# Kernel tuning notes

Hardware: AMD Instinct MI355X
Metric: run time of the kernel (lower is better)

Reference implementation:

```python
import jax, jax.numpy as jnp
import numpy as np

N = 50000
E = 1_600_000
IN = 256
OUT = 16
NEG_SLOPE = 0.2  # PyG GATConv default leaky_relu slope
EPS = 1e-16


def gat_conv(x, src, dst, W, a_src, a_dst, bias, heads, ch, concat, n_nodes):
    # Linear transform: [N, heads, ch]
    xl = (x @ W).reshape(n_nodes, heads, ch)
    # Per-node attention logits (PyG factorization of a^T [Wx_i || Wx_j])
    alpha_src = jnp.einsum('nhc,hc->nh', xl, a_src)  # [N, H]
    alpha_dst = jnp.einsum('nhc,hc->nh', xl, a_dst)  # [N, H]
    # Per-edge raw attention
    alpha = jax.nn.leaky_relu(alpha_src[src] + alpha_dst[dst], NEG_SLOPE)  # [E, H]
    # Segment softmax over incoming edges of each destination node
    amax = jax.ops.segment_max(alpha, dst, num_segments=n_nodes)  # [N, H]
    alpha = jnp.exp(alpha - amax[dst])
    denom = jax.ops.segment_sum(alpha, dst, num_segments=n_nodes)  # [N, H]
    alpha = alpha / jnp.maximum(denom[dst], EPS)
    # Weighted aggregation of source features
    msg = xl[src] * alpha[:, :, None]  # [E, H, C]
    out = jax.ops.segment_sum(msg, dst, num_segments=n_nodes)  # [N, H, C]
    out = out.reshape(n_nodes, heads * ch) if concat else out.mean(axis=1)
    return out + bias


def setup_inputs() -> dict:
    key = jax.random.key(0)
    ks = jax.random.split(key, 10)
    x = jax.random.normal(ks[0], (N, IN), dtype=jnp.float32)
    edge_index = jax.random.randint(ks[1], (2, E), 0, N, dtype=jnp.int64)
    # Layer 1: in=256 -> 8 heads x 8 ch, concat -> 64
    W1 = jax.random.normal(ks[2], (IN, 64), dtype=jnp.float32) * (1.0 / np.sqrt(IN))
    a_src1 = jax.random.normal(ks[3], (8, 8), dtype=jnp.float32) * 0.1
    a_dst1 = jax.random.normal(ks[4], (8, 8), dtype=jnp.float32) * 0.1
    b1 = jnp.zeros((64,), dtype=jnp.float32)
    # Layer 2: 64 -> 4 heads x OUT ch, mean over heads
    W2 = jax.random.normal(ks[5], (64, 4 * OUT), dtype=jnp.float32) * (1.0 / 8.0)
    a_src2 = jax.random.normal(ks[6], (4, OUT), dtype=jnp.float32) * 0.1
    a_dst2 = jax.random.normal(ks[7], (4, OUT), dtype=jnp.float32) * 0.1
    b2 = jnp.zeros((OUT,), dtype=jnp.float32)
    return {"x": x, "edge_index": edge_index, "W1": W1, "a_src1": a_src1,
            "a_dst1": a_dst1, "b1": b1, "W2": W2, "a_src2": a_src2,
            "a_dst2": a_dst2, "b2": b2}


def reference(x, edge_index, W1, a_src1, a_dst1, b1, W2, a_src2, a_dst2, b2):
    n_nodes = x.shape[0]
    # PyG GATConv adds self-loops by default
    loops = jnp.arange(n_nodes, dtype=edge_index.dtype)
    src = jnp.concatenate([edge_index[0], loops])
    dst = jnp.concatenate([edge_index[1], loops])
    # Layer 1 + ELU (dropout is identity in eval mode)
    h = jax.nn.elu(gat_conv(x, src, dst, W1, a_src1, a_dst1, b1,
                            heads=8, ch=8, concat=True, n_nodes=n_nodes))
    # Layer 2: mean over 4 heads
    out = gat_conv(h, src, dst, W2, a_src2, a_dst2, b2,
                   heads=4, ch=OUT, concat=False, n_nodes=n_nodes)
    return out
```

## Files before the change

kernel.cpp:

```cpp
#include <hip/hip_runtime.h>
#include <math.h>


#define LEAK 0.2f
#define EPSV 1e-16f
#define CHUNK 2048
#define BSH 6
#define MAXB 1024
#define LOG2E 1.44269504088896340736f

typedef __attribute__((ext_vector_type(4))) _Float16 half4;
typedef __attribute__((ext_vector_type(2))) _Float16 half2v;
typedef __attribute__((ext_vector_type(2))) __fp16 fp16v2;

#if defined(__has_builtin)
#if __has_builtin(__builtin_amdgcn_fdot2)
#define HAVE_FDOT2 1
#endif
#if __has_builtin(__builtin_amdgcn_exp2f)
#define HAVE_EXP2 1
#endif
#if __has_builtin(__builtin_amdgcn_cvt_pkrtz)
#define HAVE_PKRTZ 1
#endif
#endif

__device__ __forceinline__ float fast_exp2(float x) {
#ifdef HAVE_EXP2
    return __builtin_amdgcn_exp2f(x);
#else
    return exp2f(x);
#endif
}

__device__ __forceinline__ float elu_f(float v) {
    return (v > 0.f) ? v : (fast_exp2(v * LOG2E) - 1.f);
}

__device__ __forceinline__ half2v pack2(float a, float b) {
#ifdef HAVE_PKRTZ
    union { fp16v2 f; half2v h; } u;
    u.f = __builtin_amdgcn_cvt_pkrtz(a, b);
    return u.h;
#else
    half2v r; r.x = (_Float16)a; r.y = (_Float16)b; return r;
#endif
}

__device__ __forceinline__ half2v u2h(unsigned v) {
    union { unsigned u; half2v h; } c; c.u = v; return c.h;
}

__device__ __forceinline__ float dot2f(unsigned a, unsigned b, float c) {
    union { unsigned u; half2v h; } ua, ub;
    ua.u = a; ub.u = b;
#ifdef HAVE_FDOT2
    return __builtin_amdgcn_fdot2(ua.h, ub.h, c, false);
#else
    return fmaf((float)ua.h.x, (float)ub.h.x,
                fmaf((float)ua.h.y, (float)ub.h.y, c));
#endif
}

template<int K, int H, int CH>
__device__ __forceinline__
void nt_body(unsigned char* smem, int bid,
             const float* __restrict__ x, const float* __restrict__ W,
             const float* __restrict__ a_s, const float* __restrict__ a_d,
             _Float16* __restrict__ xl_out, float* __restrict__ asrc,
             float* __restrict__ adst, int n)
{
    _Float16 (*xsh)[72]  = reinterpret_cast<_Float16(*)[72]>(smem);
    unsigned (*wskp)[68] = reinterpret_cast<unsigned(*)[68]>(smem + 4608);
    float (*otile)[68]   = reinterpret_cast<float(*)[68]>(smem);

    int tid = threadIdx.x;
    int tx = tid & 15;
    int ty = tid >> 4;
    int nbase = bid * 32;

    float acc[2][4] = {};
    for (int k0 = 0; k0 < K; k0 += 64) {
        __syncthreads();
        #pragma unroll
        for (int rr = 0; rr < 2; ++rr) {
            int r = ty + 16 * rr;
            int node = nbase + r;
            float4 v = make_float4(0.f, 0.f, 0.f, 0.f);
            if (node < n)
                v = *reinterpret_cast<const float4*>(x + (size_t)node * K + k0 + 4 * tx);
            half4 hv;
            hv.x = (_Float16)v.x; hv.y = (_Float16)v.y;
            hv.z = (_Float16)v.z; hv.w = (_Float16)v.w;
            *reinterpret_cast<half4*>(&xsh[r][4 * tx]) = hv;
        }
        #pragma unroll
        for (int rr = 0; rr < 2; ++rr) {
            int kp = ty + 16 * rr;
            const float* w0 = W + (size_t)(k0 + 2 * kp) * 64 + 4 * tx;
            float4 wa = *reinterpret_cast<const float4*>(w0);
            float4 wb = *reinterpret_cast<const float4*>(w0 + 64);
            union { half2v h; unsigned u; } p0, p1, p2, p3;
            p0.h.x = (_Float16)wa.x; p0.h.y = (_Float16)wb.x;
            p1.h.x = (_Float16)wa.y; p1.h.y = (_Float16)wb.y;
            p2.h.x = (_Float16)wa.z; p2.h.y = (_Float16)wb.z;
            p3.h.x = (_Float16)wa.w; p3.h.y = (_Float16)wb.w;
            uint4 pk; pk.x = p0.u; pk.y = p1.u; pk.z = p2.u; pk.w = p3.u;
            *reinterpret_cast<uint4*>(&wskp[kp][4 * tx]) = pk;
        }
        __syncthreads();
        #pragma unroll 2
        for (int k8 = 0; k8 < 8; ++k8) {
            uint4 wf0 = *reinterpret_cast<const uint4*>(&wskp[k8 * 4 + 0][4 * tx]);
            uint4 wf1 = *reinterpret_cast<const uint4*>(&wskp[k8 * 4 + 1][4 * tx]);
            uint4 wf2 = *reinterpret_cast<const uint4*>(&wskp[k8 * 4 + 2][4 * tx]);
            uint4 wf3 = *reinterpret_cast<const uint4*>(&wskp[k8 * 4 + 3][4 * tx]);
            #pragma unroll
            for (int rr = 0; rr < 2; ++rr) {
                uint4 xr = *reinterpret_cast<const uint4*>(&xsh[ty + 16 * rr][k8 * 8]);
                acc[rr][0] = dot2f(xr.x, wf0.x, acc[rr][0]);
                acc[rr][1] = dot2f(xr.x, wf0.y, acc[rr][1]);
                acc[rr][2] = dot2f(xr.x, wf0.z, acc[rr][2]);
                acc[rr][3] = dot2f(xr.x, wf0.w, acc[rr][3]);
                acc[rr][0] = dot2f(xr.y, wf1.x, acc[rr][0]);
                acc[rr][1] = dot2f(xr.y, wf1.y, acc[rr][1]);
                acc[rr][2] = dot2f(xr.y, wf1.z, acc[rr][2]);
                acc[rr][3] = dot2f(xr.y, wf1.w, acc[rr][3]);
                acc[rr][0] = dot2f(xr.z, wf2.x, acc[rr][0]);
                acc[rr][1] = dot2f(xr.z, wf2.y, acc[rr][1]);
                acc[rr][2] = dot2f(xr.z, wf2.z, acc[rr][2]);
                acc[rr][3] = dot2f(xr.z, wf2.w, acc[rr][3]);
                acc[rr][0] = dot2f(xr.w, wf3.x, acc[rr][0]);
                acc[rr][1] = dot2f(xr.w, wf3.y, acc[rr][1]);
                acc[rr][2] = dot2f(xr.w, wf3.z, acc[rr][2]);
                acc[rr][3] = dot2f(xr.w, wf3.w, acc[rr][3]);
            }
        }
    }
    __syncthreads();
    #pragma unroll
    for (int rr = 0; rr < 2; ++rr) {
        int r = ty + 16 * rr;
        int node = nbase + r;
        otile[r][4 * tx + 0] = acc[rr][0];
        otile[r][4 * tx + 1] = acc[rr][1];
        otile[r][4 * tx + 2] = acc[rr][2];
        otile[r][4 * tx + 3] = acc[rr][3];
        if (node < n) {
            half4 hv;
            hv.x = (_Float16)acc[rr][0]; hv.y = (_Float16)acc[rr][1];
            hv.z = (_Float16)acc[rr][2]; hv.w = (_Float16)acc[rr][3];
            *reinterpret_cast<half4*>(xl_out + (size_t)node * 64 + 4 * tx) = hv;
        }
    }
    __syncthreads();
    for (int t = tid; t < 32 * H; t += 256) {
        int nl = t / H, h = t - nl * H;
        int node = nbase + nl;
        if (node < n) {
            float s = 0.f, d = 0.f;
            #pragma unroll
            for (int c = 0; c < CH; ++c) {
                float v = otile[nl][h * CH + c];
                s = fmaf(v, a_s[h * CH + c], s);
                d = fmaf(v, a_d[h * CH + c], d);
            }
            asrc[node * H + h] = s * LOG2E;
            adst[node * H + h] = d * LOG2E;
        }
    }
}

template<int K, int H, int CH>
__global__ __launch_bounds__(256)
void node_transform(const float* __restrict__ x, const float* __restrict__ W,
                    const float* __restrict__ a_s, const float* __restrict__ a_d,
                    _Float16* __restrict__ xl_out, float* __restrict__ asrc,
                    float* __restrict__ adst, int n)
{
    __shared__ __align__(16) unsigned char smem[13312];
    nt_body<K, H, CH>(smem, blockIdx.x, x, W, a_s, a_d, xl_out, asrc, adst, n);
}

template<int K, int H, int CH>
__global__ __launch_bounds__(256)
void nt_hist_fused(const float* __restrict__ x, const float* __restrict__ W,
                   const float* __restrict__ a_s, const float* __restrict__ a_d,
                   _Float16* __restrict__ xl_out, float* __restrict__ asrc,
                   float* __restrict__ adst, int n,
                   const int* __restrict__ dst, int E,
                   int* __restrict__ hist_mat, int NBUCK, int NSB)
{
    __shared__ __align__(16) unsigned char smem[13312];
    if ((int)blockIdx.x < NSB) {
        int* h = reinterpret_cast<int*>(smem);
        int tid = threadIdx.x, chunk = blockIdx.x;
        for (int b = tid; b < NBUCK; b += 256) h[b] = 0;
        __syncthreads();
        int base = chunk * CHUNK, end = min(base + CHUNK, E);
        for (int i = base + tid; i < end; i += 256)
            atomicAdd(&h[dst[i] >> BSH], 1);
        __syncthreads();
        for (int b = tid; b < NBUCK; b += 256)
            hist_mat[b * NSB + chunk] = h[b];
    } else {
        nt_body<K, H, CH>(smem, blockIdx.x - NSB, x, W, a_s, a_d,
                          xl_out, asrc, adst, n);
    }
}

#define SCAN_SZ 2048
__global__ __launch_bounds__(256)
void scan1_kernel(const int* __restrict__ in, int* __restrict__ part,
                  int* __restrict__ sums, int m)
{
    __shared__ int lds[256];
    int base = blockIdx.x * SCAN_SZ;
    int t = threadIdx.x;
    int v[8]; int s = 0;
    #pragma unroll
    for (int j = 0; j < 8; ++j) {
        int idx = base + t * 8 + j;
        v[j] = (idx < m) ? in[idx] : 0;
        s += v[j];
    }
    lds[t] = s;
    __syncthreads();
    for (int off = 1; off < 256; off <<= 1) {
        int a = (t >= off) ? lds[t - off] : 0;
        __syncthreads();
        lds[t] += a;
        __syncthreads();
    }
    int run = lds[t] - s;
    if (t == 255) sums[blockIdx.x] = lds[t];
    #pragma unroll
    for (int j = 0; j < 8; ++j) {
        int idx = base + t * 8 + j;
        if (idx < m) part[idx] = run;
        run += v[j];
    }
}

__global__ __launch_bounds__(256)
void scan3_kernel(const int* __restrict__ part, const int* __restrict__ sums,
                  int* __restrict__ outp, int* __restrict__ bstart,
                  int m, int NSB, int NBUCK, int E, int nb)
{
    __shared__ int spre[512];
    int i = blockIdx.x * 256 + threadIdx.x;
    if (threadIdx.x == 0) {
        int r = 0;
        for (int j = 0; j < nb; ++j) { spre[j] = r; r += sums[j]; }
    }
    __syncthreads();
    if (i < m) {
        int v = part[i] + spre[i / SCAN_SZ];
        outp[i] = v;
        if (i % NSB == 0) bstart[i / NSB] = v;
    }
    if (i == 0) bstart[NBUCK] = E;
}

__global__ __launch_bounds__(256)
void sort_place(const int* __restrict__ src, const int* __restrict__ dst, int E,
                const int* __restrict__ scanned, int NBUCK, int NSB,
                unsigned* __restrict__ ssrc)
{
    __shared__ int cur[MAXB];
    int tid = threadIdx.x, chunk = blockIdx.x;
    for (int b = tid; b < NBUCK; b += 256) cur[b] = scanned[b * NSB + chunk];
    __syncthreads();
    int base = chunk * CHUNK, end = min(base + CHUNK, E);
    for (int i = base + tid; i < end; i += 256) {
        int d = dst[i];
        int b = d >> BSH;
        int slot = atomicAdd(&cur[b], 1);
        ssrc[slot] = ((unsigned)src[i] << BSH) | (unsigned)(d & 63);
    }
}

__global__ __launch_bounds__(256)
void bucket_nodesort(const unsigned* __restrict__ ssrc, const int* __restrict__ bstart,
                     unsigned short* __restrict__ ssrc2, int* __restrict__ offs,
                     int n, int NBUCK, int E)
{
    __shared__ int cnt[64];
    __shared__ int base_[64];
    int bk = blockIdx.x, tid = threadIdx.x;
    int beg = bstart[bk], end = bstart[bk + 1];
    if (tid < 64) cnt[tid] = 0;
    __syncthreads();
    for (int i = beg + tid; i < end; i += 256)
        atomicAdd(&cnt[ssrc[i] & 63], 1);
    __syncthreads();
    if (tid == 0) {
        int r = 0;
        for (int j = 0; j < 64; ++j) { int c = cnt[j]; base_[j] = r; r += c; }
    }
    __syncthreads();
    if (tid < 64) {
        int node = (bk << BSH) + tid;
        if (node < n) offs[node] = beg + base_[tid];
        cnt[tid] = 0;
    }
    __syncthreads();
    for (int i = beg + tid; i < end; i += 256) {
        unsigned e = ssrc[i];
        int dl = e & 63;
        int r = atomicAdd(&cnt[dl], 1);
        ssrc2[beg + base_[dl] + r] = (unsigned short)(e >> BSH);
    }
    if (bk == 0 && tid == 0) offs[n] = E;
}

template<int H, int CH, int MODE>
__global__ __launch_bounds__(256)
void aggregate_csr(const int* __restrict__ offs, const unsigned short* __restrict__ ssrc2,
                   const float* __restrict__ asrc, const float* __restrict__ adst,
                   const _Float16* __restrict__ xl, const float* __restrict__ bias,
                   float* __restrict__ outp, int n)
{
    int d = blockIdx.x * 16 + (threadIdx.x >> 4);
    if (d >= n) return;
    int sub = threadIdx.x & 15;
    int g = sub >> 3;
    int s8 = sub & 7;
    int h = (s8 * 8) / CH;

    float ad = adst[(unsigned)d * H + h];
    int beg = offs[d], end = offs[d + 1];

    half2v a01 = {(_Float16)0.f, (_Float16)0.f};
    half2v a23 = a01, a45 = a01, a67 = a01;
    float den = 0.f;

    #pragma unroll 4
    for (int i = beg + g; i < end; i += 2) {
        int s = (int)ssrc2[i];
        float l = asrc[(unsigned)s * H + h] + ad;
        l = fmaxf(l, LEAK * l);
        float p = fast_exp2(l);
        uint4 hv = *reinterpret_cast<const uint4*>(xl + ((unsigned)s << 6) + 8u * s8);
        den += p;
        half2v ph = pack2(p, p);
        a01 = u2h(hv.x) * ph + a01;
        a23 = u2h(hv.y) * ph + a23;
        a45 = u2h(hv.z) * ph + a45;
        a67 = u2h(hv.w) * ph + a67;
    }

    float v8[8];
    v8[0] = (float)a01.x; v8[1] = (float)a01.y;
    v8[2] = (float)a23.x; v8[3] = (float)a23.y;
    v8[4] = (float)a45.x; v8[5] = (float)a45.y;
    v8[6] = (float)a67.x; v8[7] = (float)a67.y;
    #pragma unroll
    for (int j = 0; j < 8; ++j) v8[j] += __shfl_xor(v8[j], 8);
    den += __shfl_xor(den, 8);

    {
        float l = asrc[(unsigned)d * H + h] + ad;
        l = fmaxf(l, LEAK * l);
        float ps = fast_exp2(l);
        uint4 hv = *reinterpret_cast<const uint4*>(xl + ((unsigned)d << 6) + 8u * s8);
        den += ps;
        half2v x01 = u2h(hv.x), x23 = u2h(hv.y), x45 = u2h(hv.z), x67 = u2h(hv.w);
        v8[0] = fmaf(ps, (float)x01.x, v8[0]);
        v8[1] = fmaf(ps, (float)x01.y, v8[1]);
        v8[2] = fmaf(ps, (float)x23.x, v8[2]);
        v8[3] = fmaf(ps, (float)x23.y, v8[3]);
        v8[4] = fmaf(ps, (float)x45.x, v8[4]);
        v8[5] = fmaf(ps, (float)x45.y, v8[5]);
        v8[6] = fmaf(ps, (float)x67.x, v8[6]);
        v8[7] = fmaf(ps, (float)x67.y, v8[7]);
    }
    float inv = 1.f / fmaxf(den, EPSV);
    #pragma unroll
    for (int j = 0; j < 8; ++j) v8[j] *= inv;

    if (MODE == 1) {
        if (g == 0) {
            float4 ba = reinterpret_cast<const float4*>(bias)[2 * s8];
            float4 bb = reinterpret_cast<const float4*>(bias)[2 * s8 + 1];
            float o0 = elu_f(v8[0] + ba.x), o1 = elu_f(v8[1] + ba.y);
            float o2 = elu_f(v8[2] + ba.z), o3 = elu_f(v8[3] + ba.w);
            float o4 = elu_f(v8[4] + bb.x), o5 = elu_f(v8[5] + bb.y);
            float o6 = elu_f(v8[6] + bb.z), o7 = elu_f(v8[7] + bb.w);
            float* op = outp + (size_t)d * 64 + 8 * s8;
            *reinterpret_cast<float4*>(op)     = make_float4(o0, o1, o2, o3);
            *reinterpret_cast<float4*>(op + 4) = make_float4(o4, o5, o6, o7);
        }
    } else {
        #pragma unroll
        for (int j = 0; j < 8; ++j) {
            v8[j] += __shfl_xor(v8[j], 2);
            v8[j] += __shfl_xor(v8[j], 4);
        }
        if (sub < 2) {
            float4 ba = reinterpret_cast<const float4*>(bias)[2 * s8];
            float4 bb = reinterpret_cast<const float4*>(bias)[2 * s8 + 1];
            float* op = outp + (size_t)d * 16 + 8 * s8;
            *reinterpret_cast<float4*>(op) = make_float4(
                0.25f * v8[0] + ba.x, 0.25f * v8[1] + ba.y,
                0.25f * v8[2] + ba.z, 0.25f * v8[3] + ba.w);
            *reinterpret_cast<float4*>(op + 4) = make_float4(
                0.25f * v8[4] + bb.x, 0.25f * v8[5] + bb.y,
                0.25f * v8[6] + bb.z, 0.25f * v8[7] + bb.w);
        }
    }
}

extern "C" void kernel_launch(void* const* d_in, const int* in_sizes, int n_in,
                              void* d_out, int out_size, void* d_ws, size_t ws_size,
                              hipStream_t stream)
{
    const float* x      = (const float*)d_in[0];
    const int*   ei     = (const int*)d_in[1];
    const float* W1     = (const float*)d_in[2];
    const float* a_src1 = (const float*)d_in[3];
    const float* a_dst1 = (const float*)d_in[4];
    const float* b1     = (const float*)d_in[5];
    const float* W2     = (const float*)d_in[6];
    const float* a_src2 = (const float*)d_in[7];
    const float* a_dst2 = (const float*)d_in[8];
    const float* b2     = (const float*)d_in[9];
    float* out = (float*)d_out;

    const int n = in_sizes[0] / 256;
    const int E = in_sizes[1] / 2;
    const int* src = ei;
    const int* dst = ei + E;

    const int NSB   = (E + CHUNK - 1) / CHUNK;
    const int NBUCK = (n + 63) >> BSH;
    const int m     = NBUCK * NSB;
    const int nb    = (m + SCAN_SZ - 1) / SCAN_SZ;
    const int NTB   = (n + 31) / 32;

    size_t N64 = (size_t)n * 64;
    size_t N8  = (size_t)n * 8;
    _Float16* xlh  = (_Float16*)d_ws;
    float* hbuf    = (float*)(xlh + N64);
    float* asrc    = hbuf + N64;
    float* adst    = asrc + N8;
    int*   histm   = (int*)(adst + N8);
    int*   part    = histm + m;
    int*   scand   = part + m;
    int*   sums    = scand + m;
    int*   bstart  = sums + 512;
    int*   offs    = bstart + NBUCK + 1;
    unsigned* ssrc = (unsigned*)(offs + n + 1);
    unsigned short* ssrc2 = (unsigned short*)(ssrc + E);
    (void)ws_size; (void)n_in; (void)out_size;

    nt_hist_fused<256, 8, 8><<<NSB + NTB, 256, 0, stream>>>(
        x, W1, a_src1, a_dst1, xlh, asrc, adst, n, dst, E, histm, NBUCK, NSB);

    scan1_kernel<<<nb, 256, 0, stream>>>(histm, part, sums, m);
    scan3_kernel<<<(m + 255) / 256, 256, 0, stream>>>(part, sums, scand, bstart,
                                                      m, NSB, NBUCK, E, nb);
    sort_place<<<NSB, 256, 0, stream>>>(src, dst, E, scand, NBUCK, NSB, ssrc);
    bucket_nodesort<<<NBUCK, 256, 0, stream>>>(ssrc, bstart, ssrc2, offs, n, NBUCK, E);

    aggregate_csr<8, 8, 1><<<(n + 15) / 16, 256, 0, stream>>>(offs, ssrc2, asrc, adst,
                                                              xlh, b1, hbuf, n);

    node_transform<64, 4, 16><<<NTB, 256, 0, stream>>>(
        hbuf, W2, a_src2, a_dst2, xlh, asrc, adst, n);
    aggregate_csr<4, 16, 2><<<(n + 15) / 16, 256, 0, stream>>>(offs, ssrc2, asrc, adst,
                                                               xlh, b2, out, n);
}
```

Baseline: 159.0 us.

## Split layer-1 node transform across histogram, placement and nodesort launches

The layer-1 node transform blocks were previously all co-scheduled with the histogram kernel. They are now divided into three roughly equal thirds, each fused with one of the histogram, sort_place and bucket_nodesort kernels via block-index ranges. The goal is to fill idle CUs during the latency-bound sort phases with compute work, so the sort stages and the dense transform overlap. The cost is larger shared-memory footprints on the sort kernels and possible imbalance between the two block types.

```diff
diff --git a/kernel.cpp b/kernel.cpp
--- a/kernel.cpp
+++ b/kernel.cpp
@@ -184,12 +184,12 @@
 
 template<int K, int H, int CH>
 __global__ __launch_bounds__(256)
-void nt_hist_fused(const float* __restrict__ x, const float* __restrict__ W,
-                   const float* __restrict__ a_s, const float* __restrict__ a_d,
-                   _Float16* __restrict__ xl_out, float* __restrict__ asrc,
-                   float* __restrict__ adst, int n,
-                   const int* __restrict__ dst, int E,
-                   int* __restrict__ hist_mat, int NBUCK, int NSB)
+void hist_nt(const float* __restrict__ x, const float* __restrict__ W,
+             const float* __restrict__ a_s, const float* __restrict__ a_d,
+             _Float16* __restrict__ xl_out, float* __restrict__ asrc,
+             float* __restrict__ adst, int n,
+             const int* __restrict__ dst, int E,
+             int* __restrict__ hist_mat, int NBUCK, int NSB, int ntStart)
 {
     __shared__ __align__(16) unsigned char smem[13312];
     if ((int)blockIdx.x < NSB) {
@@ -204,8 +204,82 @@
         for (int b = tid; b < NBUCK; b += 256)
             hist_mat[b * NSB + chunk] = h[b];
     } else {
-        nt_body<K, H, CH>(smem, blockIdx.x - NSB, x, W, a_s, a_d,
-                          xl_out, asrc, adst, n);
+        nt_body<K, H, CH>(smem, ntStart + (int)blockIdx.x - NSB,
+                          x, W, a_s, a_d, xl_out, asrc, adst, n);
+    }
+}
+
+template<int K, int H, int CH>
+__global__ __launch_bounds__(256)
+void place_nt(const float* __restrict__ x, const float* __restrict__ W,
+              const float* __restrict__ a_s, const float* __restrict__ a_d,
+              _Float16* __restrict__ xl_out, float* __restrict__ asrc,
+              float* __restrict__ adst, int n,
+              const int* __restrict__ src, const int* __restrict__ dst, int E,
+              const int* __restrict__ scanned, int NBUCK, int NSB,
+              unsigned* __restrict__ ssrc, int ntStart)
+{
+    __shared__ __align__(16) unsigned char smem[13312];
+    if ((int)blockIdx.x < NSB) {
+        int* cur = reinterpret_cast<int*>(smem);
+        int tid = threadIdx.x, chunk = blockIdx.x;
+        for (int b = tid; b < NBUCK; b += 256) cur[b] = scanned[b * NSB + chunk];
+        __syncthreads();
+        int base = chunk * CHUNK, end = min(base + CHUNK, E);
+        for (int i = base + tid; i < end; i += 256) {
+            int d = dst[i];
+            int b = d >> BSH;
+            int slot = atomicAdd(&cur[b], 1);
+            ssrc[slot] = ((unsigned)src[i] << BSH) | (unsigned)(d & 63);
+        }
+    } else {
+        nt_body<K, H, CH>(smem, ntStart + (int)blockIdx.x - NSB,
+                          x, W, a_s, a_d, xl_out, asrc, adst, n);
+    }
+}
+
+template<int K, int H, int CH>
+__global__ __launch_bounds__(256)
+void nodesort_nt(const float* __restrict__ x, const float* __restrict__ W,
+                 const float* __restrict__ a_s, const float* __restrict__ a_d,
+                 _Float16* __restrict__ xl_out, float* __restrict__ asrc,
+                 float* __restrict__ adst, int n,
+                 const unsigned* __restrict__ ssrc, const int* __restrict__ bstart,
+                 unsigned short* __restrict__ ssrc2, int* __restrict__ offs,
+                 int NBUCK, int E, int ntStart)
+{
+    __shared__ __align__(16) unsigned char smem[13312];
+    if ((int)blockIdx.x < NBUCK) {
+        int* cnt  = reinterpret_cast<int*>(smem);
+        int* base_ = cnt + 64;
+        int bk = blockIdx.x, tid = threadIdx.x;
+        int beg = bstart[bk], end = bstart[bk + 1];
+        if (tid < 64) cnt[tid] = 0;
+        __syncthreads();
+        for (int i = beg + tid; i < end; i += 256)
+            atomicAdd(&cnt[ssrc[i] & 63], 1);
+        __syncthreads();
+        if (tid == 0) {
+            int r = 0;
+            for (int j = 0; j < 64; ++j) { int c = cnt[j]; base_[j] = r; r += c; }
+        }
+        __syncthreads();
+        if (tid < 64) {
+            int node = (bk << BSH) + tid;
+            if (node < n) offs[node] = beg + base_[tid];
+            cnt[tid] = 0;
+        }
+        __syncthreads();
+        for (int i = beg + tid; i < end; i += 256) {
+            unsigned e = ssrc[i];
+            int dl = e & 63;
+            int r = atomicAdd(&cnt[dl], 1);
+            ssrc2[beg + base_[dl] + r] = (unsigned short)(e >> BSH);
+        }
+        if (bk == 0 && tid == 0) offs[n] = E;
+    } else {
+        nt_body<K, H, CH>(smem, ntStart + (int)blockIdx.x - NBUCK,
+                          x, W, a_s, a_d, xl_out, asrc, adst, n);
     }
 }
 
@@ -260,58 +334,6 @@
         if (i % NSB == 0) bstart[i / NSB] = v;
     }
     if (i == 0) bstart[NBUCK] = E;
-}
-
-__global__ __launch_bounds__(256)
-void sort_place(const int* __restrict__ src, const int* __restrict__ dst, int E,
-                const int* __restrict__ scanned, int NBUCK, int NSB,
-                unsigned* __restrict__ ssrc)
-{
-    __shared__ int cur[MAXB];
-    int tid = threadIdx.x, chunk = blockIdx.x;
-    for (int b = tid; b < NBUCK; b += 256) cur[b] = scanned[b * NSB + chunk];
-    __syncthreads();
-    int base = chunk * CHUNK, end = min(base + CHUNK, E);
-    for (int i = base + tid; i < end; i += 256) {
-        int d = dst[i];
-        int b = d >> BSH;
-        int slot = atomicAdd(&cur[b], 1);
-        ssrc[slot] = ((unsigned)src[i] << BSH) | (unsigned)(d & 63);
-    }
-}
-
-__global__ __launch_bounds__(256)
-void bucket_nodesort(const unsigned* __restrict__ ssrc, const int* __restrict__ bstart,
-                     unsigned short* __restrict__ ssrc2, int* __restrict__ offs,
-                     int n, int NBUCK, int E)
-{
-    __shared__ int cnt[64];
-    __shared__ int base_[64];
-    int bk = blockIdx.x, tid = threadIdx.x;
-    int beg = bstart[bk], end = bstart[bk + 1];
-    if (tid < 64) cnt[tid] = 0;
-    __syncthreads();
-    for (int i = beg + tid; i < end; i += 256)
-        atomicAdd(&cnt[ssrc[i] & 63], 1);
-    __syncthreads();
-    if (tid == 0) {
-        int r = 0;
-        for (int j = 0; j < 64; ++j) { int c = cnt[j]; base_[j] = r; r += c; }
-    }
-    __syncthreads();
-    if (tid < 64) {
-        int node = (bk << BSH) + tid;
-        if (node < n) offs[node] = beg + base_[tid];
-        cnt[tid] = 0;
-    }
-    __syncthreads();
-    for (int i = beg + tid; i < end; i += 256) {
-        unsigned e = ssrc[i];
-        int dl = e & 63;
-        int r = atomicAdd(&cnt[dl], 1);
-        ssrc2[beg + base_[dl] + r] = (unsigned short)(e >> BSH);
-    }
-    if (bk == 0 && tid == 0) offs[n] = E;
 }
 
 template<int H, int CH, int MODE>
@@ -437,6 +459,9 @@
     const int m     = NBUCK * NSB;
     const int nb    = (m + SCAN_SZ - 1) / SCAN_SZ;
     const int NTB   = (n + 31) / 32;
+    const int T1    = NTB / 3;
+    const int T2    = NTB / 3;
+    const int T3    = NTB - T1 - T2;
 
     size_t N64 = (size_t)n * 64;
     size_t N8  = (size_t)n * 8;
@@ -454,14 +479,20 @@
     unsigned short* ssrc2 = (unsigned short*)(ssrc + E);
     (void)ws_size; (void)n_in; (void)out_size;
 
-    nt_hist_fused<256, 8, 8><<<NSB + NTB, 256, 0, stream>>>(
-        x, W1, a_src1, a_dst1, xlh, asrc, adst, n, dst, E, histm, NBUCK, NSB);
+    hist_nt<256, 8, 8><<<NSB + T1, 256, 0, stream>>>(
+        x, W1, a_src1, a_dst1, xlh, asrc, adst, n, dst, E, histm, NBUCK, NSB, 0);
 
     scan1_kernel<<<nb, 256, 0, stream>>>(histm, part, sums, m);
     scan3_kernel<<<(m + 255) / 256, 256, 0, stream>>>(part, sums, scand, bstart,
                                                       m, NSB, NBUCK, E, nb);
-    sort_place<<<NSB, 256, 0, stream>>>(src, dst, E, scand, NBUCK, NSB, ssrc);
-    bucket_nodesort<<<NBUCK, 256, 0, stream>>>(ssrc, bstart, ssrc2, offs, n, NBUCK, E);
+
+    place_nt<256, 8, 8><<<NSB + T2, 256, 0, stream>>>(
+        x, W1, a_src1, a_dst1, xlh, asrc, adst, n,
+        src, dst, E, scand, NBUCK, NSB, ssrc, T1);
+
+    nodesort_nt<256, 8, 8><<<NBUCK + T3, 256, 0, stream>>>(
+        x, W1, a_src1, a_dst1, xlh, asrc, adst, n,
+        ssrc, bstart, ssrc2, offs, NBUCK, E, T1 + T2);
 
     aggregate_csr<8, 8, 1><<<(n + 15) / 16, 256, 0, stream>>>(offs, ssrc2, asrc, adst,
                                                               xlh, b1, hbuf, n);
```

New measurement: 155.6 us. -2.1%, faster.
